# Performance work log

Measured on AMD Instinct MI355X. Metric: run time of the kernel, lower is better.

## Reference

```python
import jax, jax.numpy as jnp
import numpy as np

C = 1000          # class_num
A = 512           # feature_num
N = 65536         # batch of pooled embeddings
MOMENTUM = 0.8


def setup_inputs() -> dict:
    key = jax.random.key(0)
    k1, k2, k3, k4, k5 = jax.random.split(key, 5)
    features = jax.random.normal(k1, (N, A), dtype=jnp.float32)
    labels = jax.random.randint(k2, (N,), 0, C, dtype=jnp.int64)
    covariance = jax.random.uniform(k3, (C, A), dtype=jnp.float32)
    mean = jax.random.normal(k4, (C, A), dtype=jnp.float32)
    amount = jax.random.uniform(k5, (C,), dtype=jnp.float32) * 100.0
    return {"features": features, "labels": labels,
            "covariance": covariance, "mean": mean, "amount": amount}


def reference(features, labels, covariance, mean, amount):
    """Faithful update_diag: per-class mean/var via segment reduction instead of
    materializing the dense NxCxA onehot-masked tensor (same math)."""
    labels = labels.astype(jnp.int32)
    ones = jnp.ones((features.shape[0],), dtype=features.dtype)
    cnt = jax.ops.segment_sum(ones, labels, num_segments=C)          # [C] = onehot.sum(0)
    sums = jax.ops.segment_sum(features, labels, num_segments=C)     # [C, A]
    amount_safe = jnp.where(cnt == 0, 1.0, cnt)[:, None]             # Amount_CxA with 0 -> 1
    ave = sums / amount_safe                                          # ave_CxA
    # var_temp: masked squared deviation summed over N, / Amount
    diff2 = jnp.square(features - ave[labels])                        # [N, A]
    var = jax.ops.segment_sum(diff2, labels, num_segments=C) / amount_safe
    # weight_CV = count / (count + running amount); 0/0 -> 0
    den = cnt + amount
    w_raw = jnp.where(den > 0, cnt / jnp.where(den > 0, den, 1.0), 0.0)
    w = jnp.maximum(w_raw, 1.0 - MOMENTUM) * (w_raw > 0).astype(features.dtype)
    w = w[:, None]                                                    # [C, 1]
    additional = w * (1.0 - w) * jnp.square(mean - ave)
    new_cov = covariance * (1.0 - w) + var * w + additional
    new_mean = mean * (1.0 - w) + ave * w
    new_amount = amount + cnt
    return new_cov, new_mean, new_amount
```

## Files before the change

kernel.cpp:

```cpp
#include <hip/hip_runtime.h>

constexpr int C_ = 1000;
constexpr int A_ = 512;
constexpr int N_ = 65536;
constexpr int CA_ = C_ * A_;
constexpr float ONE_MINUS_M = 0.2f;

constexpr int TPB   = 512;
constexpr int NW    = TPB / 64;
constexpr int LPW   = N_ / NW;
constexpr int ITERS = LPW / 4 / 64;

__global__ __launch_bounds__(TPB, 8) void fused_kernel(
    const float* __restrict__ feat, const int* __restrict__ labels,
    const float* __restrict__ cov, const float* __restrict__ mean,
    const float* __restrict__ amount, float* __restrict__ out)
{
    __shared__ float lds_s[NW][A_];
    __shared__ float lds_q[NW][A_];
    __shared__ int   lds_cnt[NW];

    const int c  = blockIdx.x;
    const int wv = threadIdx.x >> 6;
    const int ln = threadIdx.x & 63;

    const int4* lab4  = reinterpret_cast<const int4*>(labels);
    const int   wbase = wv * (LPW / 4);
    const int   colb  = ln * 8;

    float4 s0 = {0,0,0,0}, s1 = {0,0,0,0};
    float4 q0 = {0,0,0,0}, q1 = {0,0,0,0};
    int cnt_w = 0;

    int4 L = lab4[wbase + ln];
    for (int it = 0; it < ITERS; ++it) {
        int4 Ln = {0,0,0,0};
        if (it + 1 < ITERS) Ln = lab4[wbase + (it + 1) * 64 + ln];

        unsigned long long m[4];
        m[0] = __ballot(L.x == c);
        m[1] = __ballot(L.y == c);
        m[2] = __ballot(L.z == c);
        m[3] = __ballot(L.w == c);
        const int rbase = (wbase + it * 64) * 4;

        #pragma unroll
        for (int comp = 0; comp < 4; ++comp) {
            unsigned long long mm = m[comp];
            cnt_w += (int)__popcll(mm);
            while (mm) {
                const int b = (int)__builtin_ctzll(mm);
                mm &= mm - 1;
                const int row = rbase + 4 * b + comp;
                const float* rp = feat + (size_t)row * A_ + colb;
                const float4 v0 = *reinterpret_cast<const float4*>(rp);
                const float4 v1 = *reinterpret_cast<const float4*>(rp + 4);
                s0.x += v0.x; s0.y += v0.y; s0.z += v0.z; s0.w += v0.w;
                s1.x += v1.x; s1.y += v1.y; s1.z += v1.z; s1.w += v1.w;
                q0.x = fmaf(v0.x, v0.x, q0.x); q0.y = fmaf(v0.y, v0.y, q0.y);
                q0.z = fmaf(v0.z, v0.z, q0.z); q0.w = fmaf(v0.w, v0.w, q0.w);
                q1.x = fmaf(v1.x, v1.x, q1.x); q1.y = fmaf(v1.y, v1.y, q1.y);
                q1.z = fmaf(v1.z, v1.z, q1.z); q1.w = fmaf(v1.w, v1.w, q1.w);
            }
        }
        L = Ln;
    }

    if (ln == 0) lds_cnt[wv] = cnt_w;
    *reinterpret_cast<float4*>(&lds_s[wv][colb])     = s0;
    *reinterpret_cast<float4*>(&lds_s[wv][colb + 4]) = s1;
    *reinterpret_cast<float4*>(&lds_q[wv][colb])     = q0;
    *reinterpret_cast<float4*>(&lds_q[wv][colb + 4]) = q1;
    __syncthreads();

    const int col = threadIdx.x;
    float s = 0.f, q = 0.f;
    #pragma unroll
    for (int w = 0; w < NW; ++w) { s += lds_s[w][col]; q += lds_q[w][col]; }
    int cntc = 0;
    #pragma unroll
    for (int w = 0; w < NW; ++w) cntc += lds_cnt[w];

    const float cntf = (float)cntc;
    const float safe = (cntc == 0) ? 1.f : cntf;
    const float inv  = 1.f / safe;
    const float ave  = s * inv;
    const float var  = fmaxf(q * inv - ave * ave, 0.f);

    const float amt   = amount[c];
    const float den   = cntf + amt;
    const float w_raw = (den > 0.f) ? (cntf / den) : 0.f;
    const float w     = (w_raw > 0.f) ? fmaxf(w_raw, ONE_MINUS_M) : 0.f;
    const float omw   = 1.f - w;

    const int idx = c * A_ + col;
    const float m  = mean[idx];
    const float cv = cov[idx];
    const float d  = m - ave;
    out[idx]       = cv * omw + var * w + w * omw * d * d;
    out[CA_ + idx] = m * omw + ave * w;
    if (col == 0) out[2 * CA_ + c] = amt + cntf;
}

extern "C" void kernel_launch(void* const* d_in, const int* in_sizes, int n_in,
                              void* d_out, int out_size, void* d_ws, size_t ws_size,
                              hipStream_t stream)
{
    const float* feat   = (const float*)d_in[0];
    const int*   labels = (const int*)  d_in[1];
    const float* cov    = (const float*)d_in[2];
    const float* mean   = (const float*)d_in[3];
    const float* amount = (const float*)d_in[4];
    float* out = (float*)d_out;

    fused_kernel<<<C_, TPB, 0, stream>>>(feat, labels, cov, mean, amount, out);
}
```

Baseline: 29.31 us.

## Process two classes per block to halve label scanning

```diff
diff --git a/kernel.cpp b/kernel.cpp
--- a/kernel.cpp
+++ b/kernel.cpp
@@ -10,8 +10,23 @@
 constexpr int NW    = TPB / 64;
 constexpr int LPW   = N_ / NW;
 constexpr int ITERS = LPW / 4 / 64;
+constexpr int NBLK  = C_ / 2;
 
-__global__ __launch_bounds__(TPB, 8) void fused_kernel(
+__device__ __forceinline__ void acc_row(const float* __restrict__ rp,
+                                        float4& s0, float4& s1,
+                                        float4& q0, float4& q1)
+{
+    const float4 v0 = *reinterpret_cast<const float4*>(rp);
+    const float4 v1 = *reinterpret_cast<const float4*>(rp + 4);
+    s0.x += v0.x; s0.y += v0.y; s0.z += v0.z; s0.w += v0.w;
+    s1.x += v1.x; s1.y += v1.y; s1.z += v1.z; s1.w += v1.w;
+    q0.x = fmaf(v0.x, v0.x, q0.x); q0.y = fmaf(v0.y, v0.y, q0.y);
+    q0.z = fmaf(v0.z, v0.z, q0.z); q0.w = fmaf(v0.w, v0.w, q0.w);
+    q1.x = fmaf(v1.x, v1.x, q1.x); q1.y = fmaf(v1.y, v1.y, q1.y);
+    q1.z = fmaf(v1.z, v1.z, q1.z); q1.w = fmaf(v1.w, v1.w, q1.w);
+}
+
+__global__ __launch_bounds__(TPB, 6) void fused_kernel(
     const float* __restrict__ feat, const int* __restrict__ labels,
     const float* __restrict__ cov, const float* __restrict__ mean,
     const float* __restrict__ amount, float* __restrict__ out)
@@ -20,7 +35,8 @@
     __shared__ float lds_q[NW][A_];
     __shared__ int   lds_cnt[NW];
 
-    const int c  = blockIdx.x;
+    const int c0 = 2 * blockIdx.x;
+    const int c1 = c0 + 1;
     const int wv = threadIdx.x >> 6;
     const int ln = threadIdx.x & 63;
 
@@ -28,78 +44,87 @@
     const int   wbase = wv * (LPW / 4);
     const int   colb  = ln * 8;
 
-    float4 s0 = {0,0,0,0}, s1 = {0,0,0,0};
-    float4 q0 = {0,0,0,0}, q1 = {0,0,0,0};
-    int cnt_w = 0;
+    float4 sA0 = {0,0,0,0}, sA1 = {0,0,0,0}, qA0 = {0,0,0,0}, qA1 = {0,0,0,0};
+    float4 sB0 = {0,0,0,0}, sB1 = {0,0,0,0}, qB0 = {0,0,0,0}, qB1 = {0,0,0,0};
+    int cntA = 0, cntB = 0;
 
     int4 L = lab4[wbase + ln];
     for (int it = 0; it < ITERS; ++it) {
         int4 Ln = {0,0,0,0};
         if (it + 1 < ITERS) Ln = lab4[wbase + (it + 1) * 64 + ln];
 
-        unsigned long long m[4];
-        m[0] = __ballot(L.x == c);
-        m[1] = __ballot(L.y == c);
-        m[2] = __ballot(L.z == c);
-        m[3] = __ballot(L.w == c);
+        const int lv[4] = {L.x, L.y, L.z, L.w};
         const int rbase = (wbase + it * 64) * 4;
 
         #pragma unroll
         for (int comp = 0; comp < 4; ++comp) {
-            unsigned long long mm = m[comp];
-            cnt_w += (int)__popcll(mm);
-            while (mm) {
-                const int b = (int)__builtin_ctzll(mm);
-                mm &= mm - 1;
-                const int row = rbase + 4 * b + comp;
-                const float* rp = feat + (size_t)row * A_ + colb;
-                const float4 v0 = *reinterpret_cast<const float4*>(rp);
-                const float4 v1 = *reinterpret_cast<const float4*>(rp + 4);
-                s0.x += v0.x; s0.y += v0.y; s0.z += v0.z; s0.w += v0.w;
-                s1.x += v1.x; s1.y += v1.y; s1.z += v1.z; s1.w += v1.w;
-                q0.x = fmaf(v0.x, v0.x, q0.x); q0.y = fmaf(v0.y, v0.y, q0.y);
-                q0.z = fmaf(v0.z, v0.z, q0.z); q0.w = fmaf(v0.w, v0.w, q0.w);
-                q1.x = fmaf(v1.x, v1.x, q1.x); q1.y = fmaf(v1.y, v1.y, q1.y);
-                q1.z = fmaf(v1.z, v1.z, q1.z); q1.w = fmaf(v1.w, v1.w, q1.w);
+            unsigned long long mA = __ballot(lv[comp] == c0);
+            unsigned long long mB = __ballot(lv[comp] == c1);
+            cntA += (int)__popcll(mA);
+            cntB += (int)__popcll(mB);
+            while (mA) {
+                const int b = (int)__builtin_ctzll(mA);
+                mA &= mA - 1;
+                acc_row(feat + (size_t)(rbase + 4 * b + comp) * A_ + colb,
+                        sA0, sA1, qA0, qA1);
+            }
+            while (mB) {
+                const int b = (int)__builtin_ctzll(mB);
+                mB &= mB - 1;
+                acc_row(feat + (size_t)(rbase + 4 * b + comp) * A_ + colb,
+                        sB0, sB1, qB0, qB1);
             }
         }
         L = Ln;
     }
 
-    if (ln == 0) lds_cnt[wv] = cnt_w;
-    *reinterpret_cast<float4*>(&lds_s[wv][colb])     = s0;
-    *reinterpret_cast<float4*>(&lds_s[wv][colb + 4]) = s1;
-    *reinterpret_cast<float4*>(&lds_q[wv][colb])     = q0;
-    *reinterpret_cast<float4*>(&lds_q[wv][colb + 4]) = q1;
-    __syncthreads();
+    #pragma unroll
+    for (int j = 0; j < 2; ++j) {
+        const int cj = (j == 0) ? c0 : c1;
+        if (ln == 0) lds_cnt[wv] = (j == 0) ? cntA : cntB;
+        if (j == 0) {
+            *reinterpret_cast<float4*>(&lds_s[wv][colb])     = sA0;
+            *reinterpret_cast<float4*>(&lds_s[wv][colb + 4]) = sA1;
+            *reinterpret_cast<float4*>(&lds_q[wv][colb])     = qA0;
+            *reinterpret_cast<float4*>(&lds_q[wv][colb + 4]) = qA1;
+        } else {
+            *reinterpret_cast<float4*>(&lds_s[wv][colb])     = sB0;
+            *reinterpret_cast<float4*>(&lds_s[wv][colb + 4]) = sB1;
+            *reinterpret_cast<float4*>(&lds_q[wv][colb])     = qB0;
+            *reinterpret_cast<float4*>(&lds_q[wv][colb + 4]) = qB1;
+        }
+        __syncthreads();
 
-    const int col = threadIdx.x;
-    float s = 0.f, q = 0.f;
-    #pragma unroll
-    for (int w = 0; w < NW; ++w) { s += lds_s[w][col]; q += lds_q[w][col]; }
-    int cntc = 0;
-    #pragma unroll
-    for (int w = 0; w < NW; ++w) cntc += lds_cnt[w];
+        const int col = threadIdx.x;
+        float s = 0.f, q = 0.f;
+        #pragma unroll
+        for (int w = 0; w < NW; ++w) { s += lds_s[w][col]; q += lds_q[w][col]; }
+        int cntc = 0;
+        #pragma unroll
+        for (int w = 0; w < NW; ++w) cntc += lds_cnt[w];
 
-    const float cntf = (float)cntc;
-    const float safe = (cntc == 0) ? 1.f : cntf;
-    const float inv  = 1.f / safe;
-    const float ave  = s * inv;
-    const float var  = fmaxf(q * inv - ave * ave, 0.f);
+        const float cntf = (float)cntc;
+        const float safe = (cntc == 0) ? 1.f : cntf;
+        const float inv  = 1.f / safe;
+        const float ave  = s * inv;
+        const float var  = fmaxf(q * inv - ave * ave, 0.f);
 
-    const float amt   = amount[c];
-    const float den   = cntf + amt;
-    const float w_raw = (den > 0.f) ? (cntf / den) : 0.f;
-    const float w     = (w_raw > 0.f) ? fmaxf(w_raw, ONE_MINUS_M) : 0.f;
-    const float omw   = 1.f - w;
+        const float amt   = amount[cj];
+        const float den   = cntf + amt;
+        const float w_raw = (den > 0.f) ? (cntf / den) : 0.f;
+        const float w     = (w_raw > 0.f) ? fmaxf(w_raw, ONE_MINUS_M) : 0.f;
+        const float omw   = 1.f - w;
 
-    const int idx = c * A_ + col;
-    const float m  = mean[idx];
-    const float cv = cov[idx];
-    const float d  = m - ave;
-    out[idx]       = cv * omw + var * w + w * omw * d * d;
-    out[CA_ + idx] = m * omw + ave * w;
-    if (col == 0) out[2 * CA_ + c] = amt + cntf;
+        const int idx = cj * A_ + col;
+        const float m  = mean[idx];
+        const float cv = cov[idx];
+        const float d  = m - ave;
+        out[idx]       = cv * omw + var * w + w * omw * d * d;
+        out[CA_ + idx] = m * omw + ave * w;
+        if (col == 0) out[2 * CA_ + cj] = amt + cntf;
+
+        __syncthreads();
+    }
 }
 
 extern "C" void kernel_launch(void* const* d_in, const int* in_sizes, int n_in,
@@ -113,5 +138,5 @@
     const float* amount = (const float*)d_in[4];
     float* out = (float*)d_out;
 
-    fused_kernel<<<C_, TPB, 0, stream>>>(feat, labels, cov, mean, amount, out);
+    fused_kernel<<<NBLK, TPB, 0, stream>>>(feat, labels, cov, mean, amount, out);
 }
```

Result: slower. 33.71 us (+15.0%).
